# Kernel tuning notes

Hardware: AMD Instinct MI355X
Metric: run time of the kernel (lower is better)

Reference implementation:

```python
import jax, jax.numpy as jnp
import numpy as np

DIM = 96; T = 3; NF = 8; HEADS = 8; GR = 32; NDL = 4; NMAB = 2; HID = 192  # hidden = dim * ffn_expansion_factor(2)
B = 2; H = 192; W = 192
EPS_LN = 1e-5
EPS_NORM = 1e-12


def conv2d(x, w, b=None, groups=1):
    # x (N,C,H,W), w (O, C//groups, kh, kw), SAME padding, stride 1
    out = jax.lax.conv_general_dilated(x, w, (1, 1), 'SAME',
                                       dimension_numbers=('NCHW', 'OIHW', 'NCHW'),
                                       feature_group_count=groups)
    if b is not None:
        out = out + b[None, :, None, None]
    return out


def conv3d_133(x, w, b=None):
    # Conv3d with kernel [1,3,3] == per-frame 2D conv. x (B,C,T,H,W)
    Bn, C, Tn, Hn, Wn = x.shape
    x2 = x.transpose(0, 2, 1, 3, 4).reshape(Bn * Tn, C, Hn, Wn)
    y = conv2d(x2, w, b)
    return y.reshape(Bn, Tn, w.shape[0], Hn, Wn).transpose(0, 2, 1, 3, 4)


def layernorm_wb(x, w, b):
    # WithBias LayerNorm over channel dim per pixel (to_3d/to_4d equivalent)
    mu = x.mean(axis=1, keepdims=True)
    var = ((x - mu) ** 2).mean(axis=1, keepdims=True)
    return (x - mu) / jnp.sqrt(var + EPS_LN) * w[None, :, None, None] + b[None, :, None, None]


def grid_sample_bilinear(img, gx, gy):
    # align_corners=True, zeros padding. img (N,C,H,W); gx,gy (N,H,W) in [-1,1]
    N, C, Hn, Wn = img.shape
    fx = (gx + 1.0) * (Wn - 1) / 2.0
    fy = (gy + 1.0) * (Hn - 1) / 2.0
    x0 = jnp.floor(fx); y0 = jnp.floor(fy)
    wx1 = fx - x0; wy1 = fy - y0

    def gat(ix, iy):
        valid = ((ix >= 0) & (ix < Wn) & (iy >= 0) & (iy < Hn)).astype(img.dtype)
        ixc = jnp.clip(ix, 0, Wn - 1).astype(jnp.int32)
        iyc = jnp.clip(iy, 0, Hn - 1).astype(jnp.int32)
        v = jax.vmap(lambda im, yy, xx: im[:, yy, xx])(img, iyc, ixc)  # (N,C,H,W)
        return v * valid[:, None]

    return (gat(x0, y0) * ((1 - wx1) * (1 - wy1))[:, None]
            + gat(x0 + 1, y0) * (wx1 * (1 - wy1))[:, None]
            + gat(x0, y0 + 1) * ((1 - wx1) * wy1)[:, None]
            + gat(x0 + 1, y0 + 1) * (wx1 * wy1)[:, None])


def backwarp(x, flow):
    # flow (N,2,H,W); per-axis scale 2/(dim-1) (same as torch code for H==W)
    N, _, Hn, Wn = flow.shape
    hor = jnp.linspace(-1.0, 1.0, Wn, dtype=flow.dtype)[None, None, :]
    ver = jnp.linspace(-1.0, 1.0, Hn, dtype=flow.dtype)[None, :, None]
    gx = hor + flow[:, 0] * (2.0 / (Wn - 1))
    gy = ver + flow[:, 1] * (2.0 / (Hn - 1))
    return grid_sample_bilinear(x, gx, gy)


def multiflow_bwarp(Fx, f):
    # Fx (b, dim, t, h, w); f (b, 3*NF, t, h, w)
    b, c, t, h, w = Fx.shape
    cd = c // NF
    Fr = Fx.reshape(b, NF, cd, t, h, w).transpose(0, 1, 3, 2, 4, 5).reshape(b * NF * t, cd, h, w)
    fr = f.reshape(b, NF, 3, t, h, w).transpose(0, 1, 3, 2, 4, 5).reshape(b * NF * t, 3, h, w)
    weight = jax.nn.sigmoid(fr[:, 2:3])
    warped = backwarp(Fr, fr[:, :2]) * weight
    return warped.reshape(b, NF, t, cd, h, w).transpose(0, 1, 3, 2, 4, 5).reshape(b, c, t, h, w)


def rdb(x, dws, cw, cb):
    # Residual dense block of [1,3,3] 3D convs (per-frame 2D)
    b, c, t, h, w = x.shape
    x2 = x.transpose(0, 2, 1, 3, 4).reshape(b * t, c, h, w)
    out = x2
    for dw in dws:
        y = jax.nn.leaky_relu(conv2d(out, dw), 0.2)
        out = jnp.concatenate([out, y], axis=1)
    out = conv2d(out, cw, cb) + x2
    return out.reshape(b, t, c, h, w).transpose(0, 2, 1, 3, 4)


def mdta_attention(x, f, temp, qkv_w, qkv_dw, proj_w):
    xin = x + f
    b, c, h, w = xin.shape
    qkv = conv2d(conv2d(xin, qkv_w), qkv_dw, groups=3 * c)
    q, k, v = jnp.split(qkv, 3, axis=1)
    hd = c // HEADS
    q = q.reshape(b, HEADS, hd, h * w)
    k = k.reshape(b, HEADS, hd, h * w)
    v = v.reshape(b, HEADS, hd, h * w)
    q = q / jnp.maximum(jnp.linalg.norm(q, axis=-1, keepdims=True), EPS_NORM)
    k = k / jnp.maximum(jnp.linalg.norm(k, axis=-1, keepdims=True), EPS_NORM)
    attn = jnp.einsum('bhcn,bhdn->bhcd', q, k) * temp[None]  # temp (HEADS,1,1)
    attn = jax.nn.softmax(attn, axis=-1)
    out = jnp.einsum('bhcd,bhdn->bhcn', attn, v).reshape(b, c, h, w)
    return conv2d(out, proj_w)


def geglu_ffn(x, pin_w, dw_w, pout_w):
    y = conv2d(x, pin_w)
    y = conv2d(y, dw_w, groups=y.shape[1])
    y1, y2 = jnp.split(y, 2, axis=1)
    return conv2d(jax.nn.gelu(y1, approximate=False) * y2, pout_w)


def setup_inputs() -> dict:
    key = jax.random.key(0)
    ks = jax.random.split(key, 20)
    s = 0.05
    inp = {
        'F': jax.random.normal(ks[0], (B, DIM, T, H, W), jnp.float32),
        'F0_c': jax.random.normal(ks[1], (B, DIM, 1, H, W), jnp.float32),
        'dense_w0': jax.random.normal(ks[2], (GR, DIM, 3, 3), jnp.float32) * s,
        'dense_w1': jax.random.normal(ks[3], (GR, DIM + GR, 3, 3), jnp.float32) * s,
        'dense_w2': jax.random.normal(ks[4], (GR, DIM + 2 * GR, 3, 3), jnp.float32) * s,
        'dense_w3': jax.random.normal(ks[5], (GR, DIM + 3 * GR, 3, 3), jnp.float32) * s,
        'rdb_conv_w': jax.random.normal(ks[6], (DIM, DIM + NDL * GR, 1, 1), jnp.float32) * s,
        'rdb_conv_b': jnp.zeros((DIM,), jnp.float32),
        'cf1_w': jax.random.normal(ks[7], (3 * NF, 2 * DIM, 3, 3), jnp.float32) * s,
        'cf2_w': jax.random.normal(ks[8], (3 * NF, 3 * NF, 3, 3), jnp.float32) * s,
        'convFw_w': jax.random.normal(ks[9], (DIM, DIM * T, 1, 1), jnp.float32) * s,
        'n1_w': jnp.ones((NMAB, DIM), jnp.float32),
        'n1_b': jnp.zeros((NMAB, DIM), jnp.float32),
        'temp': jnp.ones((NMAB, HEADS, 1, 1), jnp.float32),
        'qkv_w': jax.random.normal(ks[10], (NMAB, 3 * DIM, DIM, 1, 1), jnp.float32) * s,
        'qkv_dw_w': jax.random.normal(ks[11], (NMAB, 3 * DIM, 1, 3, 3), jnp.float32) * s,
        'proj_w': jax.random.normal(ks[12], (NMAB, DIM, DIM, 1, 1), jnp.float32) * s,
        'n2_w': jnp.ones((NMAB, DIM), jnp.float32),
        'n2_b': jnp.zeros((NMAB, DIM), jnp.float32),
        'pin_w': jax.random.normal(ks[13], (NMAB, 2 * HID, DIM, 1, 1), jnp.float32) * s,
        'ffn_dw_w': jax.random.normal(ks[14], (NMAB, 2 * HID, 1, 3, 3), jnp.float32) * s,
        'pout_w': jax.random.normal(ks[15], (NMAB, DIM, HID, 1, 1), jnp.float32) * s,
    }
    return inp


def reference(F, F0_c, dense_w0, dense_w1, dense_w2, dense_w3, rdb_conv_w, rdb_conv_b,
              cf1_w, cf2_w, convFw_w, n1_w, n1_b, temp, qkv_w, qkv_dw_w, proj_w,
              n2_w, n2_b, pin_w, ffn_dw_w, pout_w):
    Bn, C, Tn, Hn, Wn = F.shape
    Fo = rdb(F, [dense_w0, dense_w1, dense_w2, dense_w3], rdb_conv_w, rdb_conv_b)
    # first stage: f is None -> f = conv_f(cat(F0_c.repeat(T), F))
    F0_rep = jnp.broadcast_to(F0_c, (Bn, C, Tn, Hn, Wn))
    z = jnp.concatenate([F0_rep, Fo], axis=1)
    f = conv3d_133(jax.nn.leaky_relu(conv3d_133(z, cf1_w), 0.2), cf2_w)  # (B, 3*NF, T, H, W)
    warped = multiflow_bwarp(Fo, f)
    w2d = warped.reshape(Bn, C * Tn, Hn, Wn)  # 'b c t h w -> b (c t) h w'
    Fw = conv2d(w2d, convFw_w)  # Fw is None -> conv_Fw(warped)
    F0_2d = F0_c[:, :, 0]
    for i in range(NMAB):  # Kd is None (is_DA=False)
        Fw = Fw + mdta_attention(layernorm_wb(Fw, n1_w[i], n1_b[i]), F0_2d,
                                 temp[i], qkv_w[i], qkv_dw_w[i], proj_w[i])
        Fw = Fw + geglu_ffn(layernorm_wb(Fw, n2_w[i], n2_b[i]),
                            pin_w[i], ffn_dw_w[i], pout_w[i])
    return Fo, Fw, f
```

## Files before the change

### kernel.cpp

```cpp
#include <hip/hip_runtime.h>
#include <math.h>

#define HH 192
#define WW 192
#define HWQ 36864
#define NB 2
#define NT 3
#define CDIM 96

typedef __attribute__((ext_vector_type(8))) short bf16x8;
typedef __attribute__((ext_vector_type(4))) float f32x4;

__device__ __forceinline__ float lrelu02(float v){ return v > 0.f ? v : 0.2f*v; }

__device__ __forceinline__ unsigned short f2bf(float f){
    unsigned u = __builtin_bit_cast(unsigned, f);
    unsigned r = (u + 0x7fff + ((u>>16)&1)) >> 16;
    return (unsigned short)r;
}
__device__ __forceinline__ float bf2f(unsigned short u){
    unsigned v = ((unsigned)u)<<16;
    return __builtin_bit_cast(float, v);
}

__global__ __launch_bounds__(256) void k_fillcatT(const float* __restrict__ F,
                                                  unsigned short* __restrict__ catA){
    __shared__ unsigned short ls[64*104];
    const int tid = threadIdx.x;
    const int p0 = blockIdx.x*64;
    const int fi = blockIdx.z;
    const int b = fi/NT, t = fi - b*NT;
    for (int i = tid; i < 6144; i += 256){
        int px = i & 63, c = i >> 6;
        ls[px*104 + c] = f2bf(F[(((size_t)b*CDIM + c)*NT + t)*HWQ + p0 + px]);
    }
    __syncthreads();
    for (int i = tid; i < 768; i += 256){
        int px = i / 12, ck = i % 12;
        *(bf16x8*)(catA + ((size_t)fi*HWQ + p0 + px)*96 + ck*8) =
            *(const bf16x8*)(ls + px*104 + ck*8);
    }
}

__global__ __launch_bounds__(256) void k_fillF0T(const float* __restrict__ F0c,
                                                 unsigned short* __restrict__ F0T){
    __shared__ unsigned short ls[64*104];
    const int tid = threadIdx.x;
    const int p0 = blockIdx.x*64;
    const int b = blockIdx.z;
    for (int i = tid; i < 6144; i += 256){
        int px = i & 63, c = i >> 6;
        ls[px*104 + c] = f2bf(F0c[((size_t)b*96 + c)*HWQ + p0 + px]);
    }
    __syncthreads();
    for (int i = tid; i < 768; i += 256){
        int px = i / 12, ck = i % 12;
        *(bf16x8*)(F0T + ((size_t)b*HWQ + p0 + px)*96 + ck*8) =
            *(const bf16x8*)(ls + px*104 + ck*8);
    }
}

__global__ __launch_bounds__(256) void k_packF0C(const float* __restrict__ F0c,
                                                 float* __restrict__ F0C){
    __shared__ float ls[64*100];
    const int tid = threadIdx.x;
    const int p0 = blockIdx.x*64;
    const int b = blockIdx.z;
    for (int i = tid; i < 6144; i += 256){
        int px = i & 63, c = i >> 6;
        ls[px*100 + c] = F0c[((size_t)b*96 + c)*HWQ + p0 + px];
    }
    __syncthreads();
    for (int i = tid; i < 1536; i += 256){
        int px = i / 24, ck = i % 24;
        *(f32x4*)(F0C + ((size_t)b*HWQ + p0 + px)*96 + ck*4) =
            *(const f32x4*)(ls + px*100 + ck*4);
    }
}

__global__ __launch_bounds__(256) void k_unpackFw(const float* __restrict__ FwC,
                                                  float* __restrict__ Fw){
    __shared__ float ls[64*100];
    const int tid = threadIdx.x;
    const int p0 = blockIdx.x*64;
    const int b = blockIdx.z;
    for (int i = tid; i < 1536; i += 256){
        int px = i / 24, ck = i % 24;
        *(f32x4*)(ls + px*100 + ck*4) =
            *(const f32x4*)(FwC + ((size_t)b*HWQ + p0 + px)*96 + ck*4);
    }
    __syncthreads();
    for (int i = tid; i < 6144; i += 256){
        int px = i & 63, c = i >> 6;
        Fw[((size_t)b*96 + c)*HWQ + p0 + px] = ls[px*100 + c];
    }
}

__global__ __launch_bounds__(256) void k_nfsplit(const unsigned short* __restrict__ FoT,
                                                 unsigned short* __restrict__ FoT2){
    __shared__ unsigned short ls[64*104];
    const int tid = threadIdx.x;
    const int p0 = blockIdx.x*64;
    const int fi = blockIdx.z;
    const int b = fi/NT, t = fi - b*NT;
    for (int i = tid; i < 768; i += 256){
        int px = i / 12, ck = i % 12;
        *(bf16x8*)(ls + px*104 + ck*8) =
            *(const bf16x8*)(FoT + ((size_t)fi*HWQ + p0 + px)*96 + ck*8);
    }
    __syncthreads();
    for (int i = tid; i < 1536; i += 256){
        int nf = i / 192, rem = i % 192, px = rem / 3, w3 = rem % 3;
        uint2 v = *(const uint2*)(ls + px*104 + nf*12 + w3*4);
        *(uint2*)(FoT2 + (((size_t)((b*8+nf)*NT + t))*HWQ + p0 + px)*12 + w3*4) = v;
    }
}

__global__ void k_prep_dense(const float* __restrict__ w, unsigned short* __restrict__ wpk, int CIN){
    int idx = blockIdx.x*256 + threadIdx.x;
    int total = 9*CIN*32;
    if (idx >= total) return;
    int ci = idx & 31;
    int co = (idx >> 5) & 31;
    int kbtap = idx >> 10;
    int KB = CIN >> 5;
    int tap = kbtap / KB, kb = kbtap - tap*KB;
    wpk[idx] = f2bf(w[((size_t)co*CIN + kb*32 + ci)*9 + tap]);
}

__global__ void k_prep_cf1(const float* __restrict__ w, unsigned short* __restrict__ pk){
    int idx = blockIdx.x*256 + threadIdx.x;
    if (idx >= 9*6*32*32) return;
    int ci = idx & 31;
    int co = (idx >> 5) & 31;
    int tapkb = idx >> 10;
    int tap = tapkb / 6, kb = tapkb - tap*6;
    pk[idx] = (co < 24) ? f2bf(w[((size_t)co*192 + kb*32 + ci)*9 + tap]) : (unsigned short)0;
}

__global__ void k_prep_cf2(const float* __restrict__ w, unsigned short* __restrict__ pk){
    int idx = blockIdx.x*256 + threadIdx.x;
    if (idx >= 9*32*32) return;
    int ci = idx & 31;
    int co = (idx >> 5) & 31;
    int tap = idx >> 10;
    pk[idx] = (co < 24 && ci < 24) ? f2bf(w[((size_t)co*24 + ci)*9 + tap]) : (unsigned short)0;
}

struct P1Desc { const float* w; unsigned short* pk; int Cin; int Cout; };
struct P1Table { P1Desc e[11]; };
__global__ void k_prep_all1x1(P1Table tab){
    const P1Desc d = tab.e[blockIdx.y];
    int idx = blockIdx.x*256 + threadIdx.x;
    if (idx >= (d.Cin>>5)*d.Cout*32) return;
    int ci = idx & 31;
    int co = (idx >> 5) % d.Cout;
    int kb = idx / (d.Cout*32);
    d.pk[idx] = f2bf(d.w[(size_t)co*d.Cin + kb*32 + ci]);
}

template<int KB>
__global__ __launch_bounds__(256) void k_dense_mfma(const unsigned short* __restrict__ catA,
                                                    unsigned short* __restrict__ catB,
                                                    const unsigned short* __restrict__ wpk){
    __shared__ unsigned short ls[18*18*40];
    const int tid = threadIdx.x;
    const int wave = tid>>6, lane = tid&63, ln15 = lane&15, lhi = lane>>4;
    const int tile = blockIdx.x;
    const int ty = tile/12, tx = tile - ty*12;
    const int y0 = ty*16, x0 = tx*16;
    const int fi = blockIdx.z;

    f32x4 acc[4][2];
    #pragma unroll
    for (int r=0;r<4;++r){ acc[r][0]=(f32x4)(0.f); acc[r][1]=(f32x4)(0.f); }

    for (int kb=0; kb<KB; ++kb){
        const unsigned short* src;
        int cs;
        if (kb < 3){ src = catA + (size_t)fi*HWQ*96  + kb*32;      cs = 96; }
        else       { src = catB + (size_t)fi*HWQ*128 + (kb-3)*32;  cs = 128; }
        __syncthreads();
        for (int i=tid; i<1296; i+=256){
            int px = i>>2, ck = i&3;
            int iy = px/18, ix = px - iy*18;
            int gy = y0+iy-1, gx = x0+ix-1;
            bf16x8 v = (bf16x8)(short)0;
            if (gy>=0 && gy<HH && gx>=0 && gx<WW)
                v = *(const bf16x8*)(src + ((size_t)(gy*WW+gx))*cs + ck*8);
            *(bf16x8*)(ls + (px*40) + ck*8) = v;
        }
        __syncthreads();
        #pragma unroll
        for (int tap=0; tap<9; ++tap){
            const int dy = tap/3 - 1, dxk = tap - (tap/3)*3 - 1;
            const unsigned short* wb = wpk + ((size_t)(tap*KB+kb)*32)*32 + lhi*8;
            bf16x8 b0 = *(const bf16x8*)(wb + ln15*32);
            bf16x8 b1 = *(const bf16x8*)(wb + (16+ln15)*32);
            #pragma unroll
            for (int r=0;r<4;++r){
                const unsigned short* lp = ls + ((wave*4+r+dy+1)*18 + (ln15+dxk+1))*40 + lhi*8;
                bf16x8 a = *(const bf16x8*)lp;
                acc[r][0] = __builtin_amdgcn_mfma_f32_16x16x32_bf16(a, b0, acc[r][0], 0,0,0);
                acc[r][1] = __builtin_amdgcn_mfma_f32_16x16x32_bf16(a, b1, acc[r][1], 0,0,0);
            }
        }
    }
    const int coff = (KB-3)*32;
    unsigned short* ob = catB + (size_t)fi*HWQ*128;
    #pragma unroll
    for (int r=0;r<4;++r){
        const int yy = y0 + wave*4 + r;
        #pragma unroll
        for (int ct=0; ct<2; ++ct){
            const int c = coff + ct*16 + ln15;
            #pragma unroll
            for (int q=0;q<4;++q){
                const int xx = x0 + lhi*4 + q;
                ob[((size_t)(yy*WW+xx))*128 + c] = f2bf(lrelu02(acc[r][ct][q]));
            }
        }
    }
}

__global__ __launch_bounds__(256) void k_rdbfin_mfma(const unsigned short* __restrict__ catA,
                                                     const unsigned short* __restrict__ catB,
                                                     const unsigned short* __restrict__ pk,
                                                     const float* __restrict__ bias,
                                                     float* __restrict__ Fo,
                                                     unsigned short* __restrict__ FoT){
    const int tid = threadIdx.x;
    const int wave = tid>>6, lane = tid&63, ln15 = lane&15, lhi = lane>>4;
    const int tile = blockIdx.x;
    const int ty = tile/12, tx = tile - ty*12;
    const int y0 = ty*16, x0 = tx*16;
    const int fi = blockIdx.z;
    const int b = fi/NT, t = fi - b*NT;

    f32x4 acc[4][6];
    #pragma unroll
    for (int r=0;r<4;++r)
        #pragma unroll
        for (int ct=0;ct<6;++ct) acc[r][ct]=(f32x4)(0.f);

    for (int kb=0; kb<7; ++kb){
        const unsigned short* src;
        int cs;
        if (kb < 3){ src = catA + (size_t)fi*HWQ*96  + kb*32;      cs = 96; }
        else       { src = catB + (size_t)fi*HWQ*128 + (kb-3)*32;  cs = 128; }
        const unsigned short* wb = pk + ((size_t)kb*96)*32 + lhi*8;
        bf16x8 bfr[6];
        #pragma unroll
        for (int ct=0;ct<6;++ct) bfr[ct] = *(const bf16x8*)(wb + (ct*16+ln15)*32);
        #pragma unroll
        for (int r=0;r<4;++r){
            const int yy = y0 + wave*4 + r;
            const int xx = x0 + ln15;
            bf16x8 a = *(const bf16x8*)(src + ((size_t)(yy*WW+xx))*cs + lhi*8);
            #pragma unroll
            for (int ct=0;ct<6;++ct)
                acc[r][ct] = __builtin_amdgcn_mfma_f32_16x16x32_bf16(a, bfr[ct], acc[r][ct], 0,0,0);
        }
    }
    const unsigned short* resA = catA + (size_t)fi*HWQ*96;
    #pragma unroll
    for (int r=0;r<4;++r){
        const int yy = y0 + wave*4 + r;
        #pragma unroll
        for (int ct=0;ct<6;++ct){
            const int c = ct*16 + ln15;
            #pragma unroll
            for (int q=0;q<4;++q){
                const int xx = x0 + lhi*4 + q;
                float val = acc[r][ct][q] + bias[c] + bf2f(resA[((size_t)(yy*WW+xx))*96 + c]);
                Fo[(((size_t)b*CDIM + c)*NT + t)*HWQ + yy*WW + xx] = val;
                FoT[((size_t)fi*HWQ + yy*WW + xx)*96 + c] = f2bf(val);
            }
        }
    }
}

__global__ __launch_bounds__(256) void k_cf1_mfma(const unsigned short* __restrict__ F0T,
                                                  const unsigned short* __restrict__ FoT,
                                                  const unsigned short* __restrict__ pk,
                                                  unsigned short* __restrict__ t1T){
    __shared__ unsigned short ls[18*18*40];
    const int tid = threadIdx.x;
    const int wave = tid>>6, lane = tid&63, ln15 = lane&15, lhi = lane>>4;
    const int tile = blockIdx.x;
    const int ty = tile/12, tx = tile - ty*12;
    const int y0 = ty*16, x0 = tx*16;
    const int fi = blockIdx.z;
    const int b = fi/NT;
    const unsigned short* srcA = F0T + (size_t)b*HWQ*96;
    const unsigned short* srcB = FoT + (size_t)fi*HWQ*96;

    f32x4 acc[4][2];
    #pragma unroll
    for (int r=0;r<4;++r){ acc[r][0]=(f32x4)(0.f); acc[r][1]=(f32x4)(0.f); }

    for (int kb=0; kb<6; ++kb){
        const unsigned short* src = (kb<3) ? (srcA + kb*32) : (srcB + (kb-3)*32);
        __syncthreads();
        for (int i=tid; i<1296; i+=256){
            int px = i>>2, ck = i&3;
            int iy = px/18, ix = px - iy*18;
            int gy = y0+iy-1, gx = x0+ix-1;
            bf16x8 v = (bf16x8)(short)0;
            if (gy>=0 && gy<HH && gx>=0 && gx<WW)
                v = *(const bf16x8*)(src + ((size_t)(gy*WW+gx))*96 + ck*8);
            *(bf16x8*)(ls + (px*40) + ck*8) = v;
        }
        __syncthreads();
        #pragma unroll
        for (int tap=0; tap<9; ++tap){
            const int dy = tap/3 - 1, dxk = tap - (tap/3)*3 - 1;
            const unsigned short* wb = pk + ((size_t)(tap*6+kb)*32)*32 + lhi*8;
            bf16x8 b0 = *(const bf16x8*)(wb + ln15*32);
            bf16x8 b1 = *(const bf16x8*)(wb + (16+ln15)*32);
            #pragma unroll
            for (int r=0;r<4;++r){
                const unsigned short* lp = ls + ((wave*4+r+dy+1)*18 + (ln15+dxk+1))*40 + lhi*8;
                bf16x8 a = *(const bf16x8*)lp;
                acc[r][0] = __builtin_amdgcn_mfma_f32_16x16x32_bf16(a, b0, acc[r][0], 0,0,0);
                acc[r][1] = __builtin_amdgcn_mfma_f32_16x16x32_bf16(a, b1, acc[r][1], 0,0,0);
            }
        }
    }
    #pragma unroll
    for (int r=0;r<4;++r){
        const int yy = y0 + wave*4 + r;
        #pragma unroll
        for (int ct=0; ct<2; ++ct){
            const int c = ct*16 + ln15;
            #pragma unroll
            for (int q=0;q<4;++q){
                const int xx = x0 + lhi*4 + q;
                unsigned short v = (c < 24) ? f2bf(lrelu02(acc[r][ct][q])) : (unsigned short)0;
                t1T[((size_t)fi*HWQ + yy*WW + xx)*32 + c] = v;
            }
        }
    }
}

__global__ __launch_bounds__(256) void k_cf2_mfma(const unsigned short* __restrict__ t1T,
                                                  const unsigned short* __restrict__ pk,
                                                  float* __restrict__ fout){
    const int tid = threadIdx.x;
    const int wave = tid>>6, lane = tid&63, ln15 = lane&15, lhi = lane>>4;
    const int tile = blockIdx.x;
    const int ty = tile/12, tx = tile - ty*12;
    const int y0 = ty*16, x0 = tx*16;
    const int fi = blockIdx.z;
    const int b = fi/NT, t = fi - b*NT;
    const unsigned short* src = t1T + (size_t)fi*HWQ*32;

    f32x4 acc[4][2];
    #pragma unroll
    for (int r=0;r<4;++r){ acc[r][0]=(f32x4)(0.f); acc[r][1]=(f32x4)(0.f); }

    #pragma unroll
    for (int tap=0; tap<9; ++tap){
        const int dy = tap/3 - 1, dxk = tap - (tap/3)*3 - 1;
        const unsigned short* wb = pk + ((size_t)tap*32)*32 + lhi*8;
        bf16x8 b0 = *(const bf16x8*)(wb + ln15*32);
        bf16x8 b1 = *(const bf16x8*)(wb + (16+ln15)*32);
        const int xx = x0 + ln15 + dxk;
        const bool okx = (xx>=0) && (xx<WW);
        #pragma unroll
        for (int r=0;r<4;++r){
            const int yy = y0 + wave*4 + r + dy;
            bf16x8 a = (bf16x8)(short)0;
            if (okx && yy>=0 && yy<HH)
                a = *(const bf16x8*)(src + ((size_t)(yy*WW+xx))*32 + lhi*8);
            acc[r][0] = __builtin_amdgcn_mfma_f32_16x16x32_bf16(a, b0, acc[r][0], 0,0,0);
            acc[r][1] = __builtin_amdgcn_mfma_f32_16x16x32_bf16(a, b1, acc[r][1], 0,0,0);
        }
    }
    #pragma unroll
    for (int r=0;r<4;++r){
        const int yy = y0 + wave*4 + r;
        #pragma unroll
        for (int ct=0; ct<2; ++ct){
            const int c = ct*16 + ln15;
            if (c < 24){
                #pragma unroll
                for (int q=0;q<4;++q){
                    const int xx = x0 + lhi*4 + q;
                    fout[(((size_t)b*24 + c)*NT + t)*HWQ + yy*WW + xx] = acc[r][ct][q];
                }
            }
        }
    }
}

__global__ void k_bwarpcl(const unsigned short* __restrict__ FoT2, const float* __restrict__ fflow,
                          unsigned short* __restrict__ warpedT){
    int p = blockIdx.x*256 + threadIdx.x;
    int y = p/WW, x = p - y*WW;
    int nf = blockIdx.y;
    int b  = blockIdx.z;
    unsigned short* orow = warpedT + ((size_t)b*HWQ + p)*288;
    unsigned short tmp[36] __attribute__((aligned(16)));
    #pragma unroll
    for (int t=0; t<NT; ++t){
        size_t fbi = (((size_t)b*24 + nf*3)*NT + t)*HWQ + p;
        float fx = fflow[fbi];
        float fy = fflow[fbi + (size_t)NT*HWQ];
        float fwv= fflow[fbi + (size_t)2*NT*HWQ];
        float wgt = 1.f/(1.f + expf(-fwv));
        float fxp = (float)x + fx;
        float fyp = (float)y + fy;
        float x0f = floorf(fxp), y0f = floorf(fyp);
        int x0 = (int)x0f, y0 = (int)y0f;
        int x1 = x0+1,    y1 = y0+1;
        float wx1 = fxp - x0f, wy1 = fyp - y0f;
        float wx0 = 1.f - wx1, wy0 = 1.f - wy1;
        bool okx0 = (x0>=0)&&(x0<WW), okx1 = (x1>=0)&&(x1<WW);
        bool oky0 = (y0>=0)&&(y0<HH), oky1 = (y1>=0)&&(y1<HH);
        int xc0 = x0<0?0:(x0>WW-1?WW-1:x0);
        int xc1 = x1<0?0:(x1>WW-1?WW-1:x1);
        int yc0 = y0<0?0:(y0>HH-1?HH-1:y0);
        int yc1 = y1<0?0:(y1>HH-1?HH-1:y1);
        float w00 = wx0*wy0 * ((okx0&&oky0)?1.f:0.f);
        float w10 = wx1*wy0 * ((okx1&&oky0)?1.f:0.f);
        float w01 = wx0*wy1 * ((okx0&&oky1)?1.f:0.f);
        float w11 = wx1*wy1 * ((okx1&&oky1)?1.f:0.f);
        const unsigned short* fo = FoT2 + ((size_t)((b*8+nf)*NT + t))*HWQ*12;
        const unsigned short* r00 = fo + (size_t)(yc0*WW+xc0)*12;
        const unsigned short* r10 = fo + (size_t)(yc0*WW+xc1)*12;
        const unsigned short* r01 = fo + (size_t)(yc1*WW+xc0)*12;
        const unsigned short* r11 = fo + (size_t)(yc1*WW+xc1)*12;
        #pragma unroll
        for (int c=0;c<12;++c){
            float v = w00*bf2f(r00[c]) + w10*bf2f(r10[c]) + w01*bf2f(r01[c]) + w11*bf2f(r11[c]);
            tmp[c*3 + t] = f2bf(v * wgt);
        }
    }
    const uint2* ts = (const uint2*)tmp;
    uint2* td = (uint2*)(orow + nf*36);
    #pragma unroll
    for (int k=0;k<9;++k) td[k] = ts[k];
}

template<int KB, int CT, int MODE>
__global__ __launch_bounds__(256) void k_gemm_cl(const unsigned short* __restrict__ inT,
                                                 const unsigned short* __restrict__ pk,
                                                 float* __restrict__ outF,
                                                 unsigned short* __restrict__ outB,
                                                 int Ctot){
    const int tid = threadIdx.x;
    const int wave = tid>>6, lane = tid&63, ln15 = lane&15, lhi = lane>>4;
    const int px0 = blockIdx.x*256 + wave*64;
    const int og  = blockIdx.y;
    const int b   = blockIdx.z;
    const int c0  = og*CT*16;

    f32x4 acc[4][CT];
    #pragma unroll
    for (int r=0;r<4;++r)
        #pragma unroll
        for (int ct=0;ct<CT;++ct) acc[r][ct]=(f32x4)(0.f);

    for (int kb=0; kb<KB; ++kb){
        bf16x8 bfr[CT];
        #pragma unroll
        for (int ct=0;ct<CT;++ct)
            bfr[ct] = *(const bf16x8*)(pk + ((size_t)kb*Ctot + c0 + ct*16 + ln15)*32 + lhi*8);
        #pragma unroll
        for (int r=0;r<4;++r){
            const int px = px0 + r*16 + ln15;
            bf16x8 a = *(const bf16x8*)(inT + ((size_t)b*HWQ + px)*(KB*32) + kb*32 + lhi*8);
            #pragma unroll
            for (int ct=0;ct<CT;++ct)
                acc[r][ct] = __builtin_amdgcn_mfma_f32_16x16x32_bf16(a, bfr[ct], acc[r][ct], 0,0,0);
        }
    }
    #pragma unroll
    for (int r=0;r<4;++r){
        #pragma unroll
        for (int ct=0;ct<CT;++ct){
            const int c = c0 + ct*16 + ln15;
            #pragma unroll
            for (int q=0;q<4;++q){
                const int px = px0 + r*16 + lhi*4 + q;
                size_t o = ((size_t)b*HWQ + px)*Ctot + c;
                if (MODE==0) outF[o] = acc[r][ct][q];
                else if (MODE==1) outF[o] += acc[r][ct][q];
                else outB[o] = f2bf(acc[r][ct][q]);
            }
        }
    }
}

__global__ __launch_bounds__(256) void k_ln_cl(const float* __restrict__ FwC, const float* __restrict__ wln,
                        const float* __restrict__ bln, const float* __restrict__ F0C,
                        unsigned short* __restrict__ xinT){
    __shared__ float ls1[64*100];
    __shared__ float ls3[64*100];
    __shared__ unsigned short ls2[64*104];
    const int tid = threadIdx.x;
    const int p0 = blockIdx.x*64;
    const int b = blockIdx.z;
    for (int i = tid; i < 1536; i += 256){
        int px = i/24, ck = i%24;
        *(f32x4*)(ls1 + px*100 + ck*4) =
            *(const f32x4*)(FwC + ((size_t)b*HWQ + p0 + px)*96 + ck*4);
    }
    if (F0C){
        for (int i = tid; i < 1536; i += 256){
            int px = i/24, ck = i%24;
            *(f32x4*)(ls3 + px*100 + ck*4) =
                *(const f32x4*)(F0C + ((size_t)b*HWQ + p0 + px)*96 + ck*4);
        }
    }
    __syncthreads();
    const int px = tid>>2, sub = tid&3;
    float v[24];
    float s=0.f, ss=0.f;
    #pragma unroll
    for (int k=0;k<24;++k){
        v[k] = ls1[px*100 + sub*24 + k];
        s += v[k]; ss = fmaf(v[k],v[k],ss);
    }
    s  += __shfl_xor(s,1,64);  s  += __shfl_xor(s,2,64);
    ss += __shfl_xor(ss,1,64); ss += __shfl_xor(ss,2,64);
    float mu  = s*(1.f/96.f);
    float var = ss*(1.f/96.f) - mu*mu;
    float rstd = rsqrtf(var + 1e-5f);
    #pragma unroll
    for (int k=0;k<24;++k){
        int c = sub*24 + k;
        float r = (v[k]-mu)*rstd*wln[c] + bln[c];
        if (F0C) r += ls3[px*100 + c];
        ls2[px*104 + c] = f2bf(r);
    }
    __syncthreads();
    for (int i = tid; i < 768; i += 256){
        int px2 = i/12, ck = i%12;
        *(bf16x8*)(xinT + ((size_t)b*HWQ + p0 + px2)*96 + ck*8) =
            *(const bf16x8*)(ls2 + px2*104 + ck*8);
    }
}

template<int CGIN, int CGOUT, bool GATE>
__global__ __launch_bounds__(256) void k_dw2(const unsigned short* __restrict__ in,
                                             const float* __restrict__ w,
                                             unsigned short* __restrict__ outp){
    __shared__ float lw[GATE ? 576 : 288];
    const int tid = threadIdx.x;
    const int NW = GATE ? 576 : 288;
    for (int i = tid; i < NW; i += 256){
        int st = 0, j = i;
        if (GATE && j >= 288){ st = 1; j -= 288; }
        int cgi = j/72, e = (j%72)/9, tap = j%9;
        int c = (blockIdx.y*4+cgi)*8 + e + (st ? CGOUT*8 : 0);
        lw[i] = w[(size_t)c*9 + tap];
    }
    __syncthreads();
    const int xi = tid & 63, cgi = tid >> 6;
    const int xt = blockIdx.x / 24, ys = blockIdx.x % 24;
    const int x = xt*64 + xi;
    const int y0 = ys*8;
    const int cg = blockIdx.y*4 + cgi;
    const int b = blockIdx.z;
    const unsigned short* ib = in + (size_t)b*HWQ*(CGIN*8) + cg*8;
    unsigned short* ob = outp + (size_t)b*HWQ*(CGOUT*8) + cg*8;
    const float* lw1 = lw + cgi*72;
    const float* lw2 = GATE ? (lw + 288 + cgi*72) : lw;

    const bool okxm = (x-1 >= 0), okxp = (x+1 < WW);
    bf16x8 wA[3][3], wB[3][3];
    #pragma unroll
    for (int s=0;s<3;++s)
        #pragma unroll
        for (int d=0;d<3;++d){ wA[s][d]=(bf16x8)(short)0; if(GATE) wB[s][d]=(bf16x8)(short)0; }

    #pragma unroll
    for (int L=0; L<2; ++L){
        int yy = y0 + L - 1;
        if (yy >= 0){
            const unsigned short* prow = ib + ((size_t)(yy*WW))*(CGIN*8);
            #pragma unroll
            for (int d=0; d<3; ++d){
                int xx = x + d - 1;
                bool ok = (d==0) ? okxm : ((d==2) ? okxp : true);
                if (ok){
                    const unsigned short* p = prow + (size_t)xx*(CGIN*8);
                    wA[L][d] = *(const bf16x8*)p;
                    if (GATE) wB[L][d] = *(const bf16x8*)(p + CGOUT*8);
                }
            }
        }
    }
    #pragma unroll
    for (int yy=0; yy<8; ++yy){
        {
            const int sl = (yy+2)%3;
            int yr = y0 + yy + 1;
            bool oky = (yr < HH);
            #pragma unroll
            for (int d=0; d<3; ++d){
                bf16x8 v = (bf16x8)(short)0, v2 = (bf16x8)(short)0;
                bool ok = oky && ((d==0) ? okxm : ((d==2) ? okxp : true));
                if (ok){
                    const unsigned short* p = ib + ((size_t)(yr*WW + x + d - 1))*(CGIN*8);
                    v = *(const bf16x8*)p;
                    if (GATE) v2 = *(const bf16x8*)(p + CGOUT*8);
                }
                wA[sl][d] = v;
                if (GATE) wB[sl][d] = v2;
            }
        }
        float a1[8], a2[8];
        #pragma unroll
        for (int e=0;e<8;++e){ a1[e]=0.f; a2[e]=0.f; }
        #pragma unroll
        for (int dy=0; dy<3; ++dy){
            const int sl = (yy+dy)%3;
            #pragma unroll
            for (int d=0; d<3; ++d){
                bf16x8 v = wA[sl][d];
                #pragma unroll
                for (int e=0;e<8;++e)
                    a1[e] = fmaf(bf2f((unsigned short)v[e]), lw1[e*9 + dy*3 + d], a1[e]);
                if (GATE){
                    bf16x8 u = wB[sl][d];
                    #pragma unroll
                    for (int e=0;e<8;++e)
                        a2[e] = fmaf(bf2f((unsigned short)u[e]), lw2[e*9 + dy*3 + d], a2[e]);
                }
            }
        }
        bf16x8 o;
        #pragma unroll
        for (int e=0;e<8;++e){
            float r;
            if (GATE){
                float ge = 0.5f*a1[e]*(1.f + erff(a1[e]*0.70710678118654752f));
                r = ge*a2[e];
            } else r = a1[e];
            o[e] = (short)f2bf(r);
        }
        *(bf16x8*)(ob + ((size_t)((y0+yy)*WW + x))*(CGOUT*8)) = o;
    }
}

__global__ __launch_bounds__(256) void k_attnP1(const unsigned short* __restrict__ qkv2T,
                                                float* __restrict__ Spart){
    const int chunk = blockIdx.x;
    const int bh = blockIdx.y;
    const int b = bh>>3, h = bh&7;
    const int tid = threadIdx.x;
    float sq[12], sk[12], S[12][12];
    #pragma unroll
    for (int i=0;i<12;++i){ sq[i]=0.f; sk[i]=0.f;
        #pragma unroll
        for (int j=0;j<12;++j) S[i][j]=0.f; }
    for (int p = chunk*2304 + tid; p < (chunk+1)*2304; p += 256){
        const unsigned short* row = qkv2T + ((size_t)b*HWQ + p)*288;
        float q[12], k[12];
        #pragma unroll
        for (int c=0;c<12;++c){ q[c]=bf2f(row[h*12+c]); k[c]=bf2f(row[96+h*12+c]); }
        #pragma unroll
        for (int c=0;c<12;++c){ sq[c]=fmaf(q[c],q[c],sq[c]); sk[c]=fmaf(k[c],k[c],sk[c]); }
        #pragma unroll
        for (int i=0;i<12;++i)
            #pragma unroll
            for (int j=0;j<12;++j) S[i][j] = fmaf(q[i],k[j],S[i][j]);
    }
    __shared__ float red[4*168];
    const int lane = tid&63, wv = tid>>6;
    #pragma unroll
    for (int c=0;c<12;++c){
        float v = sq[c];
        v += __shfl_down(v,32,64); v += __shfl_down(v,16,64); v += __shfl_down(v,8,64);
        v += __shfl_down(v,4,64);  v += __shfl_down(v,2,64);  v += __shfl_down(v,1,64);
        if (lane==0) red[wv*168 + c] = v;
        float u = sk[c];
        u += __shfl_down(u,32,64); u += __shfl_down(u,16,64); u += __shfl_down(u,8,64);
        u += __shfl_down(u,4,64);  u += __shfl_down(u,2,64);  u += __shfl_down(u,1,64);
        if (lane==0) red[wv*168 + 12 + c] = u;
    }
    #pragma unroll
    for (int i=0;i<12;++i)
        #pragma unroll
        for (int j=0;j<12;++j){
            float v = S[i][j];
            v += __shfl_down(v,32,64); v += __shfl_down(v,16,64); v += __shfl_down(v,8,64);
            v += __shfl_down(v,4,64);  v += __shfl_down(v,2,64);  v += __shfl_down(v,1,64);
            if (lane==0) red[wv*168 + 24 + i*12 + j] = v;
        }
    __syncthreads();
    if (tid < 168){
        float s = red[tid] + red[168+tid] + red[336+tid] + red[504+tid];
        Spart[((size_t)chunk*16 + bh)*168 + tid] = s;
    }
}

__global__ void k_attnP2(const float* __restrict__ Spart, const float* __restrict__ tempp,
                         float* __restrict__ Pbuf){
    int t = threadIdx.x;
    if (t >= 192) return;
    int bh = t/12, i = t - bh*12;
    int h = bh & 7;
    float sqq = 0.f;
    for (int ch=0; ch<16; ++ch) sqq += Spart[((size_t)ch*16+bh)*168 + i];
    float qs = 1.f / fmaxf(sqrtf(sqq), 1e-12f);
    float val[12];
    #pragma unroll
    for (int j=0;j<12;++j){
        float skk = 0.f, sv = 0.f;
        for (int ch=0; ch<16; ++ch){
            skk += Spart[((size_t)ch*16+bh)*168 + 12 + j];
            sv  += Spart[((size_t)ch*16+bh)*168 + 24 + i*12 + j];
        }
        float ks = 1.f / fmaxf(sqrtf(skk), 1e-12f);
        val[j] = sv * qs * ks * tempp[h];
    }
    float mx = val[0];
    #pragma unroll
    for (int j=1;j<12;++j) mx = fmaxf(mx, val[j]);
    float sum = 0.f;
    #pragma unroll
    for (int j=0;j<12;++j){ val[j] = expf(val[j]-mx); sum += val[j]; }
    float inv = 1.f/sum;
    #pragma unroll
    for (int j=0;j<12;++j) Pbuf[(size_t)bh*144 + i*12 + j] = val[j]*inv;
}

__global__ void k_attnV2(const unsigned short* __restrict__ qkv2T, const float* __restrict__ Pbuf,
                         unsigned short* __restrict__ avT){
    __shared__ float P[1152];
    int b = blockIdx.z;
    for (int idx=threadIdx.x; idx<1152; idx+=256) P[idx] = Pbuf[(size_t)b*1152 + idx];
    __syncthreads();
    int p = blockIdx.x*256 + threadIdx.x;
    const unsigned short* row = qkv2T + ((size_t)b*HWQ + p)*288 + 192;
    float v[96];
    #pragma unroll
    for (int c=0;c<96;++c) v[c] = bf2f(row[c]);
    unsigned short* o = avT + ((size_t)b*HWQ + p)*96;
    #pragma unroll
    for (int h=0;h<8;++h){
        #pragma unroll
        for (int i=0;i<12;++i){
            float s = 0.f;
            #pragma unroll
            for (int j=0;j<12;++j) s = fmaf(P[(h*12+i)*12+j], v[h*12+j], s);
            o[h*12+i] = f2bf(s);
        }
    }
}

extern "C" void kernel_launch(void* const* d_in, const int* in_sizes, int n_in,
                              void* d_out, int out_size, void* d_ws, size_t ws_size,
                              hipStream_t stream){
    const float* F     = (const float*)d_in[0];
    const float* F0c   = (const float*)d_in[1];
    const float* dw0   = (const float*)d_in[2];
    const float* dw1   = (const float*)d_in[3];
    const float* dw2   = (const float*)d_in[4];
    const float* dw3   = (const float*)d_in[5];
    const float* rdbw  = (const float*)d_in[6];
    const float* rdbb  = (const float*)d_in[7];
    const float* cf1w  = (const float*)d_in[8];
    const float* cf2w  = (const float*)d_in[9];
    const float* cFww  = (const float*)d_in[10];
    const float* n1w   = (const float*)d_in[11];
    const float* n1b   = (const float*)d_in[12];
    const float* temp  = (const float*)d_in[13];
    const float* qkvw  = (const float*)d_in[14];
    const float* qkvdw = (const float*)d_in[15];
    const float* projw = (const float*)d_in[16];
    const float* n2w   = (const float*)d_in[17];
    const float* n2b   = (const float*)d_in[18];
    const float* pinw  = (const float*)d_in[19];
    const float* ffndw = (const float*)d_in[20];
    const float* poutw = (const float*)d_in[21];

    float* out = (float*)d_out;
    float* Fo  = out;
    float* Fw  = out + 21233664;
    float* fb  = out + 28311552;

    float* ws = (float*)d_ws;
    unsigned short* catA    = (unsigned short*)d_ws;
    unsigned short* catB    = (unsigned short*)(ws + 10616832);
    unsigned short* warpedT = (unsigned short*)d_ws;
    unsigned short* FoT2    = (unsigned short*)(ws + 10616832);
    unsigned short* qkvT    = (unsigned short*)d_ws;
    unsigned short* qkv2T   = (unsigned short*)(ws + 10616832);
    unsigned short* avT     = (unsigned short*)(ws + 21233664);
    unsigned short* ybufT   = (unsigned short*)d_ws;
    unsigned short* gatedT  = (unsigned short*)(ws + 14155776);
    unsigned short* FoT     = (unsigned short*)(ws + 24772608);
    float*          F0C     = ws + 24772608;
    unsigned short* xinT    = (unsigned short*)(ws + 31850496);
    unsigned short* F0T     = (unsigned short*)(ws + 35389440);
    unsigned short* t1T     = (unsigned short*)(ws + 38928384);
    float*          FwC     = ws + 35389440;
    float*          Spart   = ws + 42467328;
    float*          Pbuf    = ws + 42510336;
    unsigned short* P0      = (unsigned short*)(ws + 42512640);
    unsigned short* wpkd  = P0;
    unsigned short* rdbpk = P0 + 165888;
    unsigned short* cf1pk = P0 + 187392;
    unsigned short* cf2pk = P0 + 242688;
    unsigned short* cFwpk = P0 + 251904;
    unsigned short* qkvpk = P0 + 279552;
    unsigned short* projpk= P0 + 334848;
    unsigned short* pinpk = P0 + 353280;
    unsigned short* poutpk= P0 + 427008;

    dim3 blk(256,1,1);

    k_fillcatT <<<dim3(576,1,6),blk,0,stream>>>(F, catA);
    k_fillF0T  <<<dim3(576,1,2),blk,0,stream>>>(F0c, F0T);
    k_prep_dense<<<dim3(108,1,1),blk,0,stream>>>(dw0, wpkd,                96);
    k_prep_dense<<<dim3(144,1,1),blk,0,stream>>>(dw1, wpkd+27648,         128);
    k_prep_dense<<<dim3(180,1,1),blk,0,stream>>>(dw2, wpkd+27648+36864,   160);
    k_prep_dense<<<dim3(216,1,1),blk,0,stream>>>(dw3, wpkd+27648+36864+46080, 192);
    k_prep_cf1  <<<dim3(216,1,1),blk,0,stream>>>(cf1w, cf1pk);
    k_prep_cf2  <<<dim3(36,1,1),blk,0,stream>>>(cf2w, cf2pk);
    {
        P1Table tab;
        tab.e[0]  = { rdbw,                      rdbpk,          224,  96 };
        tab.e[1]  = { cFww,                      cFwpk,          288,  96 };
        tab.e[2]  = { qkvw,                      qkvpk,           96, 288 };
        tab.e[3]  = { qkvw + (size_t)288*96,     qkvpk + 27648,   96, 288 };
        tab.e[4]  = { projw,                     projpk,          96,  96 };
        tab.e[5]  = { projw + (size_t)96*96,     projpk + 9216,   96,  96 };
        tab.e[6]  = { pinw,                      pinpk,           96, 384 };
        tab.e[7]  = { pinw + (size_t)384*96,     pinpk + 36864,   96, 384 };
        tab.e[8]  = { poutw,                     poutpk,         192,  96 };
        tab.e[9]  = { poutw + (size_t)96*192,    poutpk + 18432, 192,  96 };
        tab.e[10] = { rdbw,                      rdbpk,          224,  96 };
        k_prep_all1x1<<<dim3(144,11,1),blk,0,stream>>>(tab);
    }

    k_dense_mfma<3><<<dim3(144,1,6),blk,0,stream>>>(catA, catB, wpkd);
    k_dense_mfma<4><<<dim3(144,1,6),blk,0,stream>>>(catA, catB, wpkd+27648);
    k_dense_mfma<5><<<dim3(144,1,6),blk,0,stream>>>(catA, catB, wpkd+27648+36864);
    k_dense_mfma<6><<<dim3(144,1,6),blk,0,stream>>>(catA, catB, wpkd+27648+36864+46080);
    k_rdbfin_mfma<<<dim3(144,1,6),blk,0,stream>>>(catA, catB, rdbpk, rdbb, Fo, FoT);

    k_cf1_mfma<<<dim3(144,1,6),blk,0,stream>>>(F0T, FoT, cf1pk, t1T);
    k_cf2_mfma<<<dim3(144,1,6),blk,0,stream>>>(t1T, cf2pk, fb);

    k_nfsplit<<<dim3(576,1,6),blk,0,stream>>>(FoT, FoT2);
    k_bwarpcl<<<dim3(144,8,2),blk,0,stream>>>(FoT2, fb, warpedT);
    k_packF0C<<<dim3(576,1,2),blk,0,stream>>>(F0c, F0C);
    k_gemm_cl<9,6,0><<<dim3(144,1,2),blk,0,stream>>>(warpedT, cFwpk, FwC, (unsigned short*)0, 96);

    for (int i=0;i<2;++i){
        k_ln_cl<<<dim3(576,1,2),blk,0,stream>>>(FwC, n1w+i*96, n1b+i*96, F0C, xinT);
        k_gemm_cl<3,6,2><<<dim3(144,3,2),blk,0,stream>>>(xinT, qkvpk + i*27648, (float*)0, qkvT, 288);
        k_dw2<36,36,false><<<dim3(72,9,2),blk,0,stream>>>(qkvT, qkvdw + (size_t)i*288*9, qkv2T);
        k_attnP1<<<dim3(16,16,1),blk,0,stream>>>(qkv2T, Spart);
        k_attnP2<<<dim3(1,1,1),blk,0,stream>>>(Spart, temp + i*8, Pbuf);
        k_attnV2<<<dim3(144,1,2),blk,0,stream>>>(qkv2T, Pbuf, avT);
        k_gemm_cl<3,6,1><<<dim3(144,1,2),blk,0,stream>>>(avT, projpk + i*9216, FwC, (unsigned short*)0, 96);

        k_ln_cl<<<dim3(576,1,2),blk,0,stream>>>(FwC, n2w+i*96, n2b+i*96, (const float*)0, xinT);
        k_gemm_cl<3,6,2><<<dim3(144,4,2),blk,0,stream>>>(xinT, pinpk + i*36864, (float*)0, ybufT, 384);
        k_dw2<48,24,true><<<dim3(72,6,2),blk,0,stream>>>(ybufT, ffndw + (size_t)i*384*9, gatedT);
        k_gemm_cl<6,6,1><<<dim3(144,1,2),blk,0,stream>>>(gatedT, poutpk + i*18432, FwC, (unsigned short*)0, 96);
    }

    k_unpackFw<<<dim3(576,1,2),blk,0,stream>>>(FwC, Fw);
}
```

Before: 1.063 ms.

## Double-buffer LDS tiles in 3x3 conv kernels and merge weight-prep launches

```diff
diff --git a/kernel.cpp b/kernel.cpp
--- a/kernel.cpp
+++ b/kernel.cpp
@@ -116,16 +116,19 @@
     }
 }
 
-__global__ void k_prep_dense(const float* __restrict__ w, unsigned short* __restrict__ wpk, int CIN){
+struct PDDesc { const float* w; unsigned short* pk; int CIN; };
+struct PDTable { PDDesc e[4]; };
+__global__ void k_prep_dense_all(PDTable tab){
+    const PDDesc d = tab.e[blockIdx.y];
     int idx = blockIdx.x*256 + threadIdx.x;
-    int total = 9*CIN*32;
+    int total = 9*d.CIN*32;
     if (idx >= total) return;
     int ci = idx & 31;
     int co = (idx >> 5) & 31;
     int kbtap = idx >> 10;
-    int KB = CIN >> 5;
+    int KB = d.CIN >> 5;
     int tap = kbtap / KB, kb = kbtap - tap*KB;
-    wpk[idx] = f2bf(w[((size_t)co*CIN + kb*32 + ci)*9 + tap]);
+    d.pk[idx] = f2bf(d.w[((size_t)co*d.CIN + kb*32 + ci)*9 + tap]);
 }
 
 __global__ void k_prep_cf1(const float* __restrict__ w, unsigned short* __restrict__ pk){
@@ -148,7 +151,7 @@
 }
 
 struct P1Desc { const float* w; unsigned short* pk; int Cin; int Cout; };
-struct P1Table { P1Desc e[11]; };
+struct P1Table { P1Desc e[10]; };
 __global__ void k_prep_all1x1(P1Table tab){
     const P1Desc d = tab.e[blockIdx.y];
     int idx = blockIdx.x*256 + threadIdx.x;
@@ -163,7 +166,7 @@
 __global__ __launch_bounds__(256) void k_dense_mfma(const unsigned short* __restrict__ catA,
                                                     unsigned short* __restrict__ catB,
                                                     const unsigned short* __restrict__ wpk){
-    __shared__ unsigned short ls[18*18*40];
+    __shared__ unsigned short ls[2][18*18*40];
     const int tid = threadIdx.x;
     const int wave = tid>>6, lane = tid&63, ln15 = lane&15, lhi = lane>>4;
     const int tile = blockIdx.x;
@@ -176,11 +179,11 @@
     for (int r=0;r<4;++r){ acc[r][0]=(f32x4)(0.f); acc[r][1]=(f32x4)(0.f); }
 
     for (int kb=0; kb<KB; ++kb){
+        unsigned short* lbuf = ls[kb&1];
         const unsigned short* src;
         int cs;
         if (kb < 3){ src = catA + (size_t)fi*HWQ*96  + kb*32;      cs = 96; }
         else       { src = catB + (size_t)fi*HWQ*128 + (kb-3)*32;  cs = 128; }
-        __syncthreads();
         for (int i=tid; i<1296; i+=256){
             int px = i>>2, ck = i&3;
             int iy = px/18, ix = px - iy*18;
@@ -188,7 +191,7 @@
             bf16x8 v = (bf16x8)(short)0;
             if (gy>=0 && gy<HH && gx>=0 && gx<WW)
                 v = *(const bf16x8*)(src + ((size_t)(gy*WW+gx))*cs + ck*8);
-            *(bf16x8*)(ls + (px*40) + ck*8) = v;
+            *(bf16x8*)(lbuf + (px*40) + ck*8) = v;
         }
         __syncthreads();
         #pragma unroll
@@ -199,7 +202,7 @@
             bf16x8 b1 = *(const bf16x8*)(wb + (16+ln15)*32);
             #pragma unroll
             for (int r=0;r<4;++r){
-                const unsigned short* lp = ls + ((wave*4+r+dy+1)*18 + (ln15+dxk+1))*40 + lhi*8;
+                const unsigned short* lp = lbuf + ((wave*4+r+dy+1)*18 + (ln15+dxk+1))*40 + lhi*8;
                 bf16x8 a = *(const bf16x8*)lp;
                 acc[r][0] = __builtin_amdgcn_mfma_f32_16x16x32_bf16(a, b0, acc[r][0], 0,0,0);
                 acc[r][1] = __builtin_amdgcn_mfma_f32_16x16x32_bf16(a, b1, acc[r][1], 0,0,0);
@@ -284,7 +287,7 @@
                                                   const unsigned short* __restrict__ FoT,
                                                   const unsigned short* __restrict__ pk,
                                                   unsigned short* __restrict__ t1T){
-    __shared__ unsigned short ls[18*18*40];
+    __shared__ unsigned short ls[2][18*18*40];
     const int tid = threadIdx.x;
     const int wave = tid>>6, lane = tid&63, ln15 = lane&15, lhi = lane>>4;
     const int tile = blockIdx.x;
@@ -300,8 +303,8 @@
     for (int r=0;r<4;++r){ acc[r][0]=(f32x4)(0.f); acc[r][1]=(f32x4)(0.f); }
 
     for (int kb=0; kb<6; ++kb){
+        unsigned short* lbuf = ls[kb&1];
         const unsigned short* src = (kb<3) ? (srcA + kb*32) : (srcB + (kb-3)*32);
-        __syncthreads();
         for (int i=tid; i<1296; i+=256){
             int px = i>>2, ck = i&3;
             int iy = px/18, ix = px - iy*18;
@@ -309,7 +312,7 @@
             bf16x8 v = (bf16x8)(short)0;
             if (gy>=0 && gy<HH && gx>=0 && gx<WW)
                 v = *(const bf16x8*)(src + ((size_t)(gy*WW+gx))*96 + ck*8);
-            *(bf16x8*)(ls + (px*40) + ck*8) = v;
+            *(bf16x8*)(lbuf + (px*40) + ck*8) = v;
         }
         __syncthreads();
         #pragma unroll
@@ -320,7 +323,7 @@
             bf16x8 b1 = *(const bf16x8*)(wb + (16+ln15)*32);
             #pragma unroll
             for (int r=0;r<4;++r){
-                const unsigned short* lp = ls + ((wave*4+r+dy+1)*18 + (ln15+dxk+1))*40 + lhi*8;
+                const unsigned short* lp = lbuf + ((wave*4+r+dy+1)*18 + (ln15+dxk+1))*40 + lhi*8;
                 bf16x8 a = *(const bf16x8*)lp;
                 acc[r][0] = __builtin_amdgcn_mfma_f32_16x16x32_bf16(a, b0, acc[r][0], 0,0,0);
                 acc[r][1] = __builtin_amdgcn_mfma_f32_16x16x32_bf16(a, b1, acc[r][1], 0,0,0);
@@ -817,10 +820,14 @@
 
     k_fillcatT <<<dim3(576,1,6),blk,0,stream>>>(F, catA);
     k_fillF0T  <<<dim3(576,1,2),blk,0,stream>>>(F0c, F0T);
-    k_prep_dense<<<dim3(108,1,1),blk,0,stream>>>(dw0, wpkd,                96);
-    k_prep_dense<<<dim3(144,1,1),blk,0,stream>>>(dw1, wpkd+27648,         128);
-    k_prep_dense<<<dim3(180,1,1),blk,0,stream>>>(dw2, wpkd+27648+36864,   160);
-    k_prep_dense<<<dim3(216,1,1),blk,0,stream>>>(dw3, wpkd+27648+36864+46080, 192);
+    {
+        PDTable dt;
+        dt.e[0] = { dw0, wpkd,                       96 };
+        dt.e[1] = { dw1, wpkd+27648,                128 };
+        dt.e[2] = { dw2, wpkd+27648+36864,          160 };
+        dt.e[3] = { dw3, wpkd+27648+36864+46080,    192 };
+        k_prep_dense_all<<<dim3(216,4,1),blk,0,stream>>>(dt);
+    }
     k_prep_cf1  <<<dim3(216,1,1),blk,0,stream>>>(cf1w, cf1pk);
     k_prep_cf2  <<<dim3(36,1,1),blk,0,stream>>>(cf2w, cf2pk);
     {
@@ -835,8 +842,7 @@
         tab.e[7]  = { pinw + (size_t)384*96,     pinpk + 36864,   96, 384 };
         tab.e[8]  = { poutw,                     poutpk,         192,  96 };
         tab.e[9]  = { poutw + (size_t)96*192,    poutpk + 18432, 192,  96 };
-        tab.e[10] = { rdbw,                      rdbpk,          224,  96 };
-        k_prep_all1x1<<<dim3(144,11,1),blk,0,stream>>>(tab);
+        k_prep_all1x1<<<dim3(144,10,1),blk,0,stream>>>(tab);
     }
 
     k_dense_mfma<3><<<dim3(144,1,6),blk,0,stream>>>(catA, catB, wpkd);
```

Measured after the change: 1.138 ms. 1.07x slower.
